# Kernel tuning notes

Measured on AMD Instinct MI355X. Metric: run time of the kernel, lower is better.

The kernel has to match this reference:

```python
import jax, jax.numpy as jnp
import numpy as np

DIM = 128
HEADS = 4
DIM_HEAD = 32
NUM_MEM = 4
H = 256
W = 256
SCALE = DIM_HEAD ** -0.5
NORM_SCALE = DIM ** 0.5


def rms_norm(x, gamma):
    # x: (c, h, w); L2-normalize over channel axis, per spatial location
    x32 = x.astype(jnp.float32)
    n = jnp.linalg.norm(x32, ord=2, axis=0)  # (h, w)
    return (x32 / n * (gamma + 1.0) * NORM_SCALE).astype(x.dtype)


def setup_inputs() -> dict:
    key = jax.random.key(0)
    k0, k1, k2, k3 = jax.random.split(key, 4)
    x = jax.random.normal(k0, (DIM, H, W), dtype=jnp.float32)
    gamma1 = jnp.zeros((DIM, 1, 1), dtype=jnp.float32)
    w_qkv = jax.random.normal(k1, (3 * HEADS * DIM_HEAD, DIM), dtype=jnp.float32) * 0.05
    mem_kv = jax.random.normal(k2, (2, HEADS, DIM_HEAD, NUM_MEM), dtype=jnp.float32)
    w_out = jax.random.normal(k3, (DIM, HEADS * DIM_HEAD), dtype=jnp.float32) * 0.05
    b_out = jnp.zeros((DIM,), dtype=jnp.float32)
    gamma2 = jnp.zeros((DIM, 1, 1), dtype=jnp.float32)
    return {"x": x, "gamma1": gamma1, "w_qkv": w_qkv, "mem_kv": mem_kv,
            "w_out": w_out, "b_out": b_out, "gamma2": gamma2}


def reference(x, gamma1, w_qkv, mem_kv, w_out, b_out, gamma2):
    n = H * W
    xn = rms_norm(x, gamma1)
    # 1x1 conv == channel matmul: (3*hid, c) @ (c, h*w)
    qkv = jnp.einsum('oc,cn->on', w_qkv, xn.reshape(DIM, n))
    q, k, v = jnp.split(qkv, 3, axis=0)
    # (h*d, n) -> (h, d, n)
    q = q.reshape(HEADS, DIM_HEAD, n)
    k = k.reshape(HEADS, DIM_HEAD, n)
    v = v.reshape(HEADS, DIM_HEAD, n)
    mk, mv = mem_kv[0], mem_kv[1]  # (h, d, num_mem)
    k = jnp.concatenate([mk, k], axis=-1)  # (h, d, num_mem + n)
    v = jnp.concatenate([mv, v], axis=-1)
    # softmax over feature dim for q (global max subtract), token dim for k
    q = jax.nn.softmax((q - jnp.max(q)).astype(jnp.float32), axis=-2).astype(q.dtype)
    k = jax.nn.softmax((k - jnp.max(k)).astype(jnp.float32), axis=-1).astype(k.dtype)
    q = q * SCALE
    context = jnp.einsum('hdn,hen->hde', k, v)      # (h, d, d)
    out = jnp.einsum('hde,hdn->hen', context, q)    # (h, d, n)
    out = out.reshape(HEADS * DIM_HEAD, H, W)
    out = jnp.einsum('oc,chw->ohw', w_out, out) + b_out[:, None, None]
    return rms_norm(out, gamma2)
```

## Files before the change

### kernel.cpp

```cpp
#include <hip/hip_runtime.h>
#include <hip/hip_bf16.h>
#include <cstddef>


typedef __attribute__((ext_vector_type(8))) short short8;
typedef __attribute__((ext_vector_type(4))) float f32x4;

static constexpr int   NTOK = 65536;
static constexpr float NORM_SCALE_F = 11.313708498984761f;
static constexpr float SCALE_F      = 0.17677669529663687f;

__device__ __forceinline__ unsigned short f2bf(float f) {
  __hip_bfloat16 h = __float2bfloat16(f);
  return *reinterpret_cast<unsigned short*>(&h);
}
__device__ __forceinline__ short sbf(float f) { return (short)f2bf(f); }

__global__ __launch_bounds__(256) void k0_pack(const float* __restrict__ w_qkv,
                                               const float* __restrict__ gamma1,
                                               unsigned short* __restrict__ Wp) {
  const int id = blockIdx.x * 256 + threadIdx.x;
  const int m = id / 16384, p = id % 16384;
  const int j = p & 7, ln = (p >> 3) & 63, frag = p >> 9;
  const int ks = frag & 3, rt = frag >> 2;
  const int row = rt * 16 + (ln & 15);
  const int c = ks * 32 + (ln >> 4) * 8 + j;
  const float v = w_qkv[(m * 128 + row) * 128 + c] * (gamma1[c] + 1.0f) * NORM_SCALE_F;
  Wp[id] = f2bf(v);
}

__global__ __launch_bounds__(256) void k_norm(const float* __restrict__ x,
                                              unsigned short* __restrict__ xn) {
  const int t = threadIdx.x;
  const int tok = blockIdx.x * 64 + (t >> 2);
  const int cg = (t & 3) * 32;
  float v[32];
  float sq = 0.f;
  #pragma unroll
  for (int j = 0; j < 32; ++j) {
    v[j] = x[(size_t)(cg + j) * NTOK + tok];
    sq += v[j] * v[j];
  }
  sq += __shfl_xor(sq, 1, 64);
  sq += __shfl_xor(sq, 2, 64);
  const float s = rsqrtf(sq);
  #pragma unroll
  for (int g = 0; g < 4; ++g) {
    short8 o;
    #pragma unroll
    for (int j = 0; j < 8; ++j) o[j] = sbf(v[g * 8 + j] * s);
    *reinterpret_cast<short8*>(xn + (size_t)tok * 128 + cg + g * 8) = o;
  }
}

__global__ __launch_bounds__(512) void k1_kv(const unsigned short* __restrict__ xn,
                                             const unsigned short* __restrict__ Wkp,
                                             const unsigned short* __restrict__ Wvp,
                                             float* __restrict__ CpAll) {
  __shared__ float cred[4224];
  const int tid = threadIdx.x, wv = tid >> 6, ln = tid & 63;
  const int g4 = ln >> 4, t16 = ln & 15;
  const int n0 = (blockIdx.x * 8 + wv) * 32;

  for (int i = tid; i < 4224; i += 512) cred[i] = 0.f;
  __syncthreads();

  short8 xf[2][4];
  #pragma unroll
  for (int tg = 0; tg < 2; ++tg)
    #pragma unroll
    for (int ks = 0; ks < 4; ++ks)
      xf[tg][ks] = *reinterpret_cast<const short8*>(
          xn + (size_t)(n0 + tg * 16 + t16) * 128 + ks * 32 + g4 * 8);

  #pragma unroll
  for (int h = 0; h < 4; ++h) {
    f32x4 ka[2][2] = {};
    #pragma unroll
    for (int ks = 0; ks < 4; ++ks) {
      const short8 b0 = *reinterpret_cast<const short8*>(Wkp + (((2 * h + 0) * 4 + ks) * 64 + ln) * 8);
      const short8 b1 = *reinterpret_cast<const short8*>(Wkp + (((2 * h + 1) * 4 + ks) * 64 + ln) * 8);
      #pragma unroll
      for (int tg = 0; tg < 2; ++tg) {
        ka[0][tg] = __builtin_amdgcn_mfma_f32_16x16x32_bf16(xf[tg][ks], b0, ka[0][tg], 0, 0, 0);
        ka[1][tg] = __builtin_amdgcn_mfma_f32_16x16x32_bf16(xf[tg][ks], b1, ka[1][tg], 0, 0, 0);
      }
    }
    short8 keA[2];
    #pragma unroll
    for (int mt = 0; mt < 2; ++mt) {
      float sl = 0.f;
      short8 u;
      #pragma unroll
      for (int tg = 0; tg < 2; ++tg)
        #pragma unroll
        for (int r = 0; r < 4; ++r) {
          const float e = __expf(ka[mt][tg][r]);
          sl += e;
          u[tg * 4 + r] = sbf(e);
        }
      keA[mt] = u;
      sl += __shfl_xor(sl, 16, 64);
      sl += __shfl_xor(sl, 32, 64);
      if (g4 == 0) atomicAdd(&cred[4096 + h * 32 + mt * 16 + t16], sl);
    }
    f32x4 va[2][2] = {};
    #pragma unroll
    for (int ks = 0; ks < 4; ++ks) {
      const short8 b0 = *reinterpret_cast<const short8*>(Wvp + (((2 * h + 0) * 4 + ks) * 64 + ln) * 8);
      const short8 b1 = *reinterpret_cast<const short8*>(Wvp + (((2 * h + 1) * 4 + ks) * 64 + ln) * 8);
      #pragma unroll
      for (int tg = 0; tg < 2; ++tg) {
        va[0][tg] = __builtin_amdgcn_mfma_f32_16x16x32_bf16(xf[tg][ks], b0, va[0][tg], 0, 0, 0);
        va[1][tg] = __builtin_amdgcn_mfma_f32_16x16x32_bf16(xf[tg][ks], b1, va[1][tg], 0, 0, 0);
      }
    }
    short8 vB[2];
    #pragma unroll
    for (int et = 0; et < 2; ++et) {
      short8 u;
      #pragma unroll
      for (int tg = 0; tg < 2; ++tg)
        #pragma unroll
        for (int r = 0; r < 4; ++r)
          u[tg * 4 + r] = sbf(va[et][tg][r]);
      vB[et] = u;
    }
    #pragma unroll
    for (int dt = 0; dt < 2; ++dt)
      #pragma unroll
      for (int et = 0; et < 2; ++et) {
        f32x4 zc = {0.f, 0.f, 0.f, 0.f};
        zc = __builtin_amdgcn_mfma_f32_16x16x32_bf16(keA[dt], vB[et], zc, 0, 0, 0);
        #pragma unroll
        for (int r = 0; r < 4; ++r)
          atomicAdd(&cred[h * 1024 + (dt * 16 + g4 * 4 + r) * 32 + et * 16 + t16], zc[r]);
      }
  }

  __syncthreads();
  for (int i = tid; i < 4224; i += 512)
    CpAll[(size_t)blockIdx.x * 4224 + i] = cred[i];
}

__global__ __launch_bounds__(256) void k3a_reduce(const float* __restrict__ CpAll,
                                                  float* __restrict__ Cpp) {
  __shared__ float red[256];
  const int t = threadIdx.x;
  const int eg = blockIdx.x;
  const int ch = blockIdx.y;
  const int e = eg * 128 + (t & 127);
  const int half = t >> 7;
  float s = 0.f;
  for (int bb = 0; bb < 16; ++bb) {
    const int b = ch * 32 + half * 16 + bb;
    s += CpAll[(size_t)b * 4224 + e];
  }
  red[t] = s;
  __syncthreads();
  if (t < 128) Cpp[ch * 4224 + eg * 128 + t] = red[t] + red[t + 128];
}

__global__ __launch_bounds__(256) void k3b1_ctx(const float* __restrict__ Cpp,
                                                const float* __restrict__ mem_kv,
                                                float* __restrict__ ctx) {
  __shared__ float allv[4224];
  const int t = threadIdx.x;
  for (int e = t; e < 4224; e += 256) {
    float s = 0.f;
    #pragma unroll
    for (int c = 0; c < 8; ++c) s += Cpp[c * 4224 + e];
    allv[e] = s;
  }
  __syncthreads();
  for (int e = t; e < 4224; e += 256) {
    if (e < 4096) {
      const int hh = e >> 10, d = (e >> 5) & 31, ev = e & 31;
      float add = 0.f;
      #pragma unroll
      for (int m = 0; m < 4; ++m)
        add += __expf(mem_kv[(hh * 32 + d) * 4 + m]) * mem_kv[512 + (hh * 32 + ev) * 4 + m];
      allv[e] += add;
    } else {
      const int si = e - 4096;
      const int hh = si >> 5, d = si & 31;
      float add = 0.f;
      #pragma unroll
      for (int m = 0; m < 4; ++m) add += __expf(mem_kv[(hh * 32 + d) * 4 + m]);
      allv[e] += add;
    }
  }
  __syncthreads();
  for (int e = t; e < 4096; e += 256)
    ctx[e] = allv[e] / allv[4096 + (e >> 5)];
}

__global__ __launch_bounds__(256) void k3b2_w2(const float* __restrict__ ctx,
                                               const float* __restrict__ w_out,
                                               unsigned short* __restrict__ W2p) {
  const int base = (blockIdx.x * 256 + threadIdx.x) * 8;
  const int ln = (base >> 3) & 63;
  const int frag = base >> 9;
  const int h = frag & 3, ot = frag >> 2;
  const int o = ot * 16 + (ln & 15);
  float wrow[32];
  #pragma unroll
  for (int e = 0; e < 32; ++e) wrow[e] = w_out[o * 128 + h * 32 + e];
  short8 out8;
  #pragma unroll
  for (int j = 0; j < 8; ++j) {
    const int d = (j >> 2) * 16 + ((ln >> 4) << 2) + (j & 3);
    float s = 0.f;
    #pragma unroll
    for (int e = 0; e < 32; ++e)
      s += wrow[e] * ctx[h * 1024 + d * 32 + e];
    out8[j] = sbf(s * SCALE_F);
  }
  *reinterpret_cast<short8*>(W2p + base) = out8;
}

__global__ __launch_bounds__(256) void k5_out(const unsigned short* __restrict__ xn,
                                              const unsigned short* __restrict__ Wqp,
                                              const unsigned short* __restrict__ W2p,
                                              const float* __restrict__ b_out,
                                              const float* __restrict__ gamma2,
                                              float* __restrict__ y) {
  const int tid = threadIdx.x, wv = tid >> 6, ln = tid & 63;
  const int g4 = ln >> 4, t16 = ln & 15;
  const int n0 = (blockIdx.x * 4 + wv) * 32;

  short8 xf[2][4];
  #pragma unroll
  for (int tg = 0; tg < 2; ++tg)
    #pragma unroll
    for (int ks = 0; ks < 4; ++ks)
      xf[tg][ks] = *reinterpret_cast<const short8*>(
          xn + (size_t)(n0 + tg * 16 + t16) * 128 + ks * 32 + g4 * 8);

  short8 qB[4][2];
  #pragma unroll
  for (int h = 0; h < 4; ++h) {
    f32x4 qa[2][2] = {};
    #pragma unroll
    for (int ks = 0; ks < 4; ++ks) {
      const short8 a0 = *reinterpret_cast<const short8*>(Wqp + (((2 * h + 0) * 4 + ks) * 64 + ln) * 8);
      const short8 a1 = *reinterpret_cast<const short8*>(Wqp + (((2 * h + 1) * 4 + ks) * 64 + ln) * 8);
      #pragma unroll
      for (int tg = 0; tg < 2; ++tg) {
        qa[0][tg] = __builtin_amdgcn_mfma_f32_16x16x32_bf16(a0, xf[tg][ks], qa[0][tg], 0, 0, 0);
        qa[1][tg] = __builtin_amdgcn_mfma_f32_16x16x32_bf16(a1, xf[tg][ks], qa[1][tg], 0, 0, 0);
      }
    }
    #pragma unroll
    for (int tg = 0; tg < 2; ++tg) {
      float ev[2][4];
      float ss = 0.f;
      #pragma unroll
      for (int rtl = 0; rtl < 2; ++rtl)
        #pragma unroll
        for (int r = 0; r < 4; ++r) {
          ev[rtl][r] = __expf(qa[rtl][tg][r]);
          ss += ev[rtl][r];
        }
      ss += __shfl_xor(ss, 16, 64);
      ss += __shfl_xor(ss, 32, 64);
      const float inv = 1.0f / ss;
      short8 u;
      #pragma unroll
      for (int rtl = 0; rtl < 2; ++rtl)
        #pragma unroll
        for (int r = 0; r < 4; ++r)
          u[rtl * 4 + r] = sbf(ev[rtl][r] * inv);
      qB[h][tg] = u;
    }
  }

  f32x4 z[8][2] = {};
  #pragma unroll
  for (int h = 0; h < 4; ++h)
    #pragma unroll
    for (int ot = 0; ot < 8; ++ot) {
      const short8 a = *reinterpret_cast<const short8*>(W2p + ((ot * 4 + h) * 64 + ln) * 8);
      #pragma unroll
      for (int tg = 0; tg < 2; ++tg)
        z[ot][tg] = __builtin_amdgcn_mfma_f32_16x16x32_bf16(a, qB[h][tg], z[ot][tg], 0, 0, 0);
    }

  float ssq[2] = {0.f, 0.f};
  #pragma unroll
  for (int ot = 0; ot < 8; ++ot) {
    const float4 bb = *reinterpret_cast<const float4*>(b_out + ot * 16 + g4 * 4);
    const float barr[4] = {bb.x, bb.y, bb.z, bb.w};
    #pragma unroll
    for (int tg = 0; tg < 2; ++tg)
      #pragma unroll
      for (int r = 0; r < 4; ++r) {
        const float zb = z[ot][tg][r] + barr[r];
        z[ot][tg][r] = zb;
        ssq[tg] += zb * zb;
      }
  }
  float rr[2];
  #pragma unroll
  for (int tg = 0; tg < 2; ++tg) {
    float s = ssq[tg];
    s += __shfl_xor(s, 16, 64);
    s += __shfl_xor(s, 32, 64);
    rr[tg] = rsqrtf(s);
  }
  #pragma unroll
  for (int ot = 0; ot < 8; ++ot) {
    const float4 gg = *reinterpret_cast<const float4*>(gamma2 + ot * 16 + g4 * 4);
    const float garr[4] = {gg.x, gg.y, gg.z, gg.w};
    #pragma unroll
    for (int tg = 0; tg < 2; ++tg)
      #pragma unroll
      for (int r = 0; r < 4; ++r) {
        const int row = ot * 16 + g4 * 4 + r;
        y[(size_t)row * NTOK + n0 + tg * 16 + t16] =
            z[ot][tg][r] * rr[tg] * (garr[r] + 1.0f) * NORM_SCALE_F;
      }
  }
}

extern "C" void kernel_launch(void* const* d_in, const int* in_sizes, int n_in,
                              void* d_out, int out_size, void* d_ws, size_t ws_size,
                              hipStream_t stream) {
  const float* x      = (const float*)d_in[0];
  const float* gamma1 = (const float*)d_in[1];
  const float* w_qkv  = (const float*)d_in[2];
  const float* mem_kv = (const float*)d_in[3];
  const float* w_out  = (const float*)d_in[4];
  const float* b_out  = (const float*)d_in[5];
  const float* gamma2 = (const float*)d_in[6];
  float* out = (float*)d_out;
  float* ws  = (float*)d_ws;

  unsigned short* Wqp = (unsigned short*)ws;
  unsigned short* Wkp = Wqp + 16384;
  unsigned short* Wvp = Wkp + 16384;
  unsigned short* W2p = Wvp + 16384;
  float* CpAll = ws + 32768;
  float* Cpp   = CpAll + 1081344;
  float* ctx   = Cpp + 33792;
  unsigned short* xn = (unsigned short*)(ws + 1152000);

  hipLaunchKernelGGL(k0_pack,    dim3(192),    dim3(256), 0, stream, w_qkv, gamma1, Wqp);
  hipLaunchKernelGGL(k_norm,     dim3(1024),   dim3(256), 0, stream, x, xn);
  hipLaunchKernelGGL(k1_kv,      dim3(256),    dim3(512), 0, stream, xn, Wkp, Wvp, CpAll);
  hipLaunchKernelGGL(k3a_reduce, dim3(33, 8),  dim3(256), 0, stream, CpAll, Cpp);
  hipLaunchKernelGGL(k3b1_ctx,   dim3(1),      dim3(256), 0, stream, Cpp, mem_kv, ctx);
  hipLaunchKernelGGL(k3b2_w2,    dim3(8),      dim3(256), 0, stream, ctx, w_out, W2p);
  hipLaunchKernelGGL(k5_out,     dim3(512),    dim3(256), 0, stream, xn, Wqp, W2p, b_out, gamma2, out);
}
```

Baseline: 182.3 us.

## Fuse all stages into one cooperative persistent kernel with grid syncs

Replaces the seven-kernel pipeline with a single cooperative kernel of 256 blocks that keeps each block's normalized token tile and packed weights in shared memory across phases, using grid.sync between the reduction and context stages. This removes the xn round trip through global memory, the separate weight-pack kernels and several launch gaps. It also accumulates context partials in registers before doing shared atomics once. In exchange, grid-wide barriers serialize the small reduction phases and leave most threads idle during them, and occupancy is limited by the large shared-memory footprint.

```diff
diff --git a/kernel.cpp b/kernel.cpp
--- a/kernel.cpp
+++ b/kernel.cpp
@@ -1,6 +1,9 @@
 #include <hip/hip_runtime.h>
 #include <hip/hip_bf16.h>
+#include <hip/hip_cooperative_groups.h>
 #include <cstddef>
+
+namespace cg = cooperative_groups;
 
 
 typedef __attribute__((ext_vector_type(8))) short short8;
@@ -16,52 +19,65 @@
 }
 __device__ __forceinline__ short sbf(float f) { return (short)f2bf(f); }
 
-__global__ __launch_bounds__(256) void k0_pack(const float* __restrict__ w_qkv,
-                                               const float* __restrict__ gamma1,
-                                               unsigned short* __restrict__ Wp) {
-  const int id = blockIdx.x * 256 + threadIdx.x;
-  const int m = id / 16384, p = id % 16384;
-  const int j = p & 7, ln = (p >> 3) & 63, frag = p >> 9;
-  const int ks = frag & 3, rt = frag >> 2;
-  const int row = rt * 16 + (ln & 15);
-  const int c = ks * 32 + (ln >> 4) * 8 + j;
-  const float v = w_qkv[(m * 128 + row) * 128 + c] * (gamma1[c] + 1.0f) * NORM_SCALE_F;
-  Wp[id] = f2bf(v);
-}
-
-__global__ __launch_bounds__(256) void k_norm(const float* __restrict__ x,
-                                              unsigned short* __restrict__ xn) {
-  const int t = threadIdx.x;
-  const int tok = blockIdx.x * 64 + (t >> 2);
-  const int cg = (t & 3) * 32;
-  float v[32];
-  float sq = 0.f;
-  #pragma unroll
-  for (int j = 0; j < 32; ++j) {
-    v[j] = x[(size_t)(cg + j) * NTOK + tok];
-    sq += v[j] * v[j];
-  }
-  sq += __shfl_xor(sq, 1, 64);
-  sq += __shfl_xor(sq, 2, 64);
-  const float s = rsqrtf(sq);
-  #pragma unroll
-  for (int g = 0; g < 4; ++g) {
+#define MFMA16(A, B, C) __builtin_amdgcn_mfma_f32_16x16x32_bf16((A), (B), (C), 0, 0, 0)
+
+__global__ __launch_bounds__(512, 2) void k_all(
+    const float* __restrict__ x, const float* __restrict__ gamma1,
+    const float* __restrict__ w_qkv, const float* __restrict__ mem_kv,
+    const float* __restrict__ w_out, const float* __restrict__ b_out,
+    const float* __restrict__ gamma2, float* __restrict__ y,
+    float* __restrict__ CpAll, float* __restrict__ Cpp,
+    float* __restrict__ ctxN, unsigned short* __restrict__ W2p) {
+  __shared__ unsigned short xbuf[256 * 136];
+  __shared__ unsigned short wbuf[32768];
+  __shared__ float cred[4224];
+
+  cg::grid_group grid = cg::this_grid();
+
+  const int tid = threadIdx.x, bid = blockIdx.x;
+  const int wv = tid >> 6, ln = tid & 63;
+  const int g4 = ln >> 4, t16 = ln & 15;
+  const int tok0 = bid * 256;
+
+  #pragma unroll
+  for (int g = 0; g < 8; ++g) {
+    const int gi = tid * 8 + g;
+    const int m = 1 + (gi >> 11);
+    const int gg = gi & 2047;
+    const int lnp = gg & 63, frag = gg >> 6;
+    const int ks = frag & 3, rt = frag >> 2;
+    const int row = rt * 16 + (lnp & 15);
+    const int cb = ks * 32 + (lnp >> 4) * 8;
     short8 o;
     #pragma unroll
-    for (int j = 0; j < 8; ++j) o[j] = sbf(v[g * 8 + j] * s);
-    *reinterpret_cast<short8*>(xn + (size_t)tok * 128 + cg + g * 8) = o;
-  }
-}
-
-__global__ __launch_bounds__(512) void k1_kv(const unsigned short* __restrict__ xn,
-                                             const unsigned short* __restrict__ Wkp,
-                                             const unsigned short* __restrict__ Wvp,
-                                             float* __restrict__ CpAll) {
-  __shared__ float cred[4224];
-  const int tid = threadIdx.x, wv = tid >> 6, ln = tid & 63;
-  const int g4 = ln >> 4, t16 = ln & 15;
-  const int n0 = (blockIdx.x * 8 + wv) * 32;
-
+    for (int j = 0; j < 8; ++j)
+      o[j] = sbf(w_qkv[(m * 128 + row) * 128 + cb + j] * (gamma1[cb + j] + 1.0f) * NORM_SCALE_F);
+    *reinterpret_cast<short8*>(&wbuf[gi * 8]) = o;
+  }
+
+  #pragma unroll
+  for (int it = 0; it < 2; ++it) {
+    const int j = it * 512 + tid;
+    const int tl = j >> 2;
+    const int cgs = (j & 3) * 32;
+    float v[32];
+    float sq = 0.f;
+    #pragma unroll
+    for (int jj = 0; jj < 32; ++jj) {
+      v[jj] = x[(size_t)(cgs + jj) * NTOK + tok0 + tl];
+      sq += v[jj] * v[jj];
+    }
+    sq += __shfl_xor(sq, 1, 64);
+    sq += __shfl_xor(sq, 2, 64);
+    const float s = rsqrtf(sq);
+    #pragma unroll
+    for (int g = 0; g < 4; ++g) {
+      short8 o;
+      #pragma unroll
+      for (int jj = 0; jj < 8; ++jj) o[jj] = sbf(v[g * 8 + jj] * s);
+      *reinterpret_cast<short8*>(&xbuf[tl * 136 + cgs + g * 8]) = o;
+    }
+  }
   for (int i = tid; i < 4224; i += 512) cred[i] = 0.f;
   __syncthreads();
 
@@ -71,184 +87,184 @@
     #pragma unroll
     for (int ks = 0; ks < 4; ++ks)
       xf[tg][ks] = *reinterpret_cast<const short8*>(
-          xn + (size_t)(n0 + tg * 16 + t16) * 128 + ks * 32 + g4 * 8);
-
-  #pragma unroll
-  for (int h = 0; h < 4; ++h) {
-    f32x4 ka[2][2] = {};
-    #pragma unroll
-    for (int ks = 0; ks < 4; ++ks) {
-      const short8 b0 = *reinterpret_cast<const short8*>(Wkp + (((2 * h + 0) * 4 + ks) * 64 + ln) * 8);
-      const short8 b1 = *reinterpret_cast<const short8*>(Wkp + (((2 * h + 1) * 4 + ks) * 64 + ln) * 8);
-      #pragma unroll
-      for (int tg = 0; tg < 2; ++tg) {
-        ka[0][tg] = __builtin_amdgcn_mfma_f32_16x16x32_bf16(xf[tg][ks], b0, ka[0][tg], 0, 0, 0);
-        ka[1][tg] = __builtin_amdgcn_mfma_f32_16x16x32_bf16(xf[tg][ks], b1, ka[1][tg], 0, 0, 0);
-      }
-    }
-    short8 keA[2];
-    #pragma unroll
-    for (int mt = 0; mt < 2; ++mt) {
-      float sl = 0.f;
-      short8 u;
-      #pragma unroll
-      for (int tg = 0; tg < 2; ++tg)
-        #pragma unroll
-        for (int r = 0; r < 4; ++r) {
-          const float e = __expf(ka[mt][tg][r]);
-          sl += e;
-          u[tg * 4 + r] = sbf(e);
+          &xbuf[(wv * 32 + tg * 16 + t16) * 136 + ks * 32 + g4 * 8]);
+
+  {
+    f32x4 cacc[4][2][2] = {};
+    float sacc[4][2] = {};
+    #pragma unroll
+    for (int h = 0; h < 4; ++h) {
+      f32x4 ka[2][2] = {};
+      #pragma unroll
+      for (int ks = 0; ks < 4; ++ks) {
+        const short8 b0 = *reinterpret_cast<const short8*>(&wbuf[(((2 * h + 0) * 4 + ks) * 64 + ln) * 8]);
+        const short8 b1 = *reinterpret_cast<const short8*>(&wbuf[(((2 * h + 1) * 4 + ks) * 64 + ln) * 8]);
+        #pragma unroll
+        for (int tg = 0; tg < 2; ++tg) {
+          ka[0][tg] = MFMA16(xf[tg][ks], b0, ka[0][tg]);
+          ka[1][tg] = MFMA16(xf[tg][ks], b1, ka[1][tg]);
         }
-      keA[mt] = u;
-      sl += __shfl_xor(sl, 16, 64);
-      sl += __shfl_xor(sl, 32, 64);
-      if (g4 == 0) atomicAdd(&cred[4096 + h * 32 + mt * 16 + t16], sl);
-    }
-    f32x4 va[2][2] = {};
-    #pragma unroll
-    for (int ks = 0; ks < 4; ++ks) {
-      const short8 b0 = *reinterpret_cast<const short8*>(Wvp + (((2 * h + 0) * 4 + ks) * 64 + ln) * 8);
-      const short8 b1 = *reinterpret_cast<const short8*>(Wvp + (((2 * h + 1) * 4 + ks) * 64 + ln) * 8);
-      #pragma unroll
-      for (int tg = 0; tg < 2; ++tg) {
-        va[0][tg] = __builtin_amdgcn_mfma_f32_16x16x32_bf16(xf[tg][ks], b0, va[0][tg], 0, 0, 0);
-        va[1][tg] = __builtin_amdgcn_mfma_f32_16x16x32_bf16(xf[tg][ks], b1, va[1][tg], 0, 0, 0);
-      }
-    }
-    short8 vB[2];
-    #pragma unroll
-    for (int et = 0; et < 2; ++et) {
-      short8 u;
-      #pragma unroll
-      for (int tg = 0; tg < 2; ++tg)
-        #pragma unroll
-        for (int r = 0; r < 4; ++r)
-          u[tg * 4 + r] = sbf(va[et][tg][r]);
-      vB[et] = u;
-    }
-    #pragma unroll
-    for (int dt = 0; dt < 2; ++dt)
+      }
+      short8 keA[2];
+      #pragma unroll
+      for (int mt = 0; mt < 2; ++mt) {
+        float sl = 0.f;
+        short8 u;
+        #pragma unroll
+        for (int tg = 0; tg < 2; ++tg)
+          #pragma unroll
+          for (int r = 0; r < 4; ++r) {
+            const float e = __expf(ka[mt][tg][r]);
+            sl += e;
+            u[tg * 4 + r] = sbf(e);
+          }
+        keA[mt] = u;
+        sacc[h][mt] += sl;
+      }
+      f32x4 va[2][2] = {};
+      #pragma unroll
+      for (int ks = 0; ks < 4; ++ks) {
+        const short8 b0 = *reinterpret_cast<const short8*>(&wbuf[16384 + (((2 * h + 0) * 4 + ks) * 64 + ln) * 8]);
+        const short8 b1 = *reinterpret_cast<const short8*>(&wbuf[16384 + (((2 * h + 1) * 4 + ks) * 64 + ln) * 8]);
+        #pragma unroll
+        for (int tg = 0; tg < 2; ++tg) {
+          va[0][tg] = MFMA16(xf[tg][ks], b0, va[0][tg]);
+          va[1][tg] = MFMA16(xf[tg][ks], b1, va[1][tg]);
+        }
+      }
+      short8 vB[2];
       #pragma unroll
       for (int et = 0; et < 2; ++et) {
-        f32x4 zc = {0.f, 0.f, 0.f, 0.f};
-        zc = __builtin_amdgcn_mfma_f32_16x16x32_bf16(keA[dt], vB[et], zc, 0, 0, 0);
-        #pragma unroll
-        for (int r = 0; r < 4; ++r)
-          atomicAdd(&cred[h * 1024 + (dt * 16 + g4 * 4 + r) * 32 + et * 16 + t16], zc[r]);
-      }
-  }
-
+        short8 u;
+        #pragma unroll
+        for (int tg = 0; tg < 2; ++tg)
+          #pragma unroll
+          for (int r = 0; r < 4; ++r)
+            u[tg * 4 + r] = sbf(va[et][tg][r]);
+        vB[et] = u;
+      }
+      #pragma unroll
+      for (int dt = 0; dt < 2; ++dt)
+        #pragma unroll
+        for (int et = 0; et < 2; ++et)
+          cacc[h][dt][et] = MFMA16(keA[dt], vB[et], cacc[h][dt][et]);
+    }
+    #pragma unroll
+    for (int h = 0; h < 4; ++h)
+      #pragma unroll
+      for (int dt = 0; dt < 2; ++dt)
+        #pragma unroll
+        for (int et = 0; et < 2; ++et)
+          #pragma unroll
+          for (int r = 0; r < 4; ++r)
+            atomicAdd(&cred[h * 1024 + (dt * 16 + g4 * 4 + r) * 32 + et * 16 + t16],
+                      cacc[h][dt][et][r]);
+    #pragma unroll
+    for (int h = 0; h < 4; ++h)
+      #pragma unroll
+      for (int mt = 0; mt < 2; ++mt) {
+        float sl = sacc[h][mt];
+        sl += __shfl_xor(sl, 16, 64);
+        sl += __shfl_xor(sl, 32, 64);
+        if (g4 == 0) atomicAdd(&cred[4096 + h * 32 + mt * 16 + t16], sl);
+      }
+  }
   __syncthreads();
   for (int i = tid; i < 4224; i += 512)
-    CpAll[(size_t)blockIdx.x * 4224 + i] = cred[i];
-}
-
-__global__ __launch_bounds__(256) void k3a_reduce(const float* __restrict__ CpAll,
-                                                  float* __restrict__ Cpp) {
-  __shared__ float red[256];
-  const int t = threadIdx.x;
-  const int eg = blockIdx.x;
-  const int ch = blockIdx.y;
-  const int e = eg * 128 + (t & 127);
-  const int half = t >> 7;
-  float s = 0.f;
-  for (int bb = 0; bb < 16; ++bb) {
-    const int b = ch * 32 + half * 16 + bb;
-    s += CpAll[(size_t)b * 4224 + e];
-  }
-  red[t] = s;
+    CpAll[(size_t)bid * 4224 + i] = cred[i];
+  __threadfence();
+  grid.sync();
+
+  const int gid = bid * 512 + tid;
+  if (gid < 33792) {
+    const unsigned chunk = (unsigned)gid / 4224u;
+    const unsigned e = (unsigned)gid - chunk * 4224u;
+    float s = 0.f;
+    #pragma unroll 4
+    for (int bb = 0; bb < 32; ++bb)
+      s += CpAll[(size_t)(chunk * 32 + bb) * 4224 + e];
+    Cpp[chunk * 4224 + e] = s;
+  }
+  #pragma unroll
+  for (int g = 0; g < 4; ++g) {
+    const int gi = tid * 4 + g;
+    const int lnp = gi & 63, frag = gi >> 6;
+    const int ks = frag & 3, rt = frag >> 2;
+    const int row = rt * 16 + (lnp & 15);
+    const int cb = ks * 32 + (lnp >> 4) * 8;
+    short8 o;
+    #pragma unroll
+    for (int j = 0; j < 8; ++j)
+      o[j] = sbf(w_qkv[row * 128 + cb + j] * (gamma1[cb + j] + 1.0f) * NORM_SCALE_F);
+    *reinterpret_cast<short8*>(&wbuf[gi * 8]) = o;
+  }
+  __threadfence();
+  grid.sync();
+
+  if (gid < 4224) {
+    float s = 0.f;
+    #pragma unroll
+    for (int c = 0; c < 8; ++c) s += Cpp[c * 4224 + gid];
+    if (gid < 4096) {
+      const int hh = gid >> 10, d = (gid >> 5) & 31, ev = gid & 31;
+      #pragma unroll
+      for (int m = 0; m < 4; ++m)
+        s += __expf(mem_kv[(hh * 32 + d) * 4 + m]) * mem_kv[512 + (hh * 32 + ev) * 4 + m];
+    } else {
+      const int si = gid - 4096;
+      const int hh = si >> 5, d = si & 31;
+      #pragma unroll
+      for (int m = 0; m < 4; ++m) s += __expf(mem_kv[(hh * 32 + d) * 4 + m]);
+    }
+    ctxN[gid] = s;
+  }
+  __threadfence();
+  grid.sync();
+
+  if (gid < 2048) {
+    const int base = gid * 8;
+    const int ln2 = gid & 63, frag = gid >> 6;
+    const int h = frag & 3, ot = frag >> 2;
+    const int o = ot * 16 + (ln2 & 15);
+    float wrow[32];
+    #pragma unroll
+    for (int e = 0; e < 32; ++e) wrow[e] = w_out[o * 128 + h * 32 + e];
+    short8 o8;
+    #pragma unroll
+    for (int j = 0; j < 8; ++j) {
+      const int d = (j >> 2) * 16 + ((ln2 >> 4) << 2) + (j & 3);
+      float s = 0.f;
+      #pragma unroll
+      for (int e = 0; e < 32; ++e)
+        s += wrow[e] * ctxN[h * 1024 + d * 32 + e];
+      o8[j] = sbf(s / ctxN[4096 + h * 32 + d] * SCALE_F);
+    }
+    *reinterpret_cast<short8*>(&W2p[base]) = o8;
+  }
+  __threadfence();
+  grid.sync();
+
+  #pragma unroll
+  for (int g = 0; g < 4; ++g) {
+    const int i8 = (tid * 4 + g) * 8;
+    *reinterpret_cast<short8*>(&wbuf[16384 + i8]) =
+        *reinterpret_cast<const short8*>(&W2p[i8]);
+  }
   __syncthreads();
-  if (t < 128) Cpp[ch * 4224 + eg * 128 + t] = red[t] + red[t + 128];
-}
-
-__global__ __launch_bounds__(256) void k3b1_ctx(const float* __restrict__ Cpp,
-                                                const float* __restrict__ mem_kv,
-                                                float* __restrict__ ctx) {
-  __shared__ float allv[4224];
-  const int t = threadIdx.x;
-  for (int e = t; e < 4224; e += 256) {
-    float s = 0.f;
-    #pragma unroll
-    for (int c = 0; c < 8; ++c) s += Cpp[c * 4224 + e];
-    allv[e] = s;
-  }
-  __syncthreads();
-  for (int e = t; e < 4224; e += 256) {
-    if (e < 4096) {
-      const int hh = e >> 10, d = (e >> 5) & 31, ev = e & 31;
-      float add = 0.f;
-      #pragma unroll
-      for (int m = 0; m < 4; ++m)
-        add += __expf(mem_kv[(hh * 32 + d) * 4 + m]) * mem_kv[512 + (hh * 32 + ev) * 4 + m];
-      allv[e] += add;
-    } else {
-      const int si = e - 4096;
-      const int hh = si >> 5, d = si & 31;
-      float add = 0.f;
-      #pragma unroll
-      for (int m = 0; m < 4; ++m) add += __expf(mem_kv[(hh * 32 + d) * 4 + m]);
-      allv[e] += add;
-    }
-  }
-  __syncthreads();
-  for (int e = t; e < 4096; e += 256)
-    ctx[e] = allv[e] / allv[4096 + (e >> 5)];
-}
-
-__global__ __launch_bounds__(256) void k3b2_w2(const float* __restrict__ ctx,
-                                               const float* __restrict__ w_out,
-                                               unsigned short* __restrict__ W2p) {
-  const int base = (blockIdx.x * 256 + threadIdx.x) * 8;
-  const int ln = (base >> 3) & 63;
-  const int frag = base >> 9;
-  const int h = frag & 3, ot = frag >> 2;
-  const int o = ot * 16 + (ln & 15);
-  float wrow[32];
-  #pragma unroll
-  for (int e = 0; e < 32; ++e) wrow[e] = w_out[o * 128 + h * 32 + e];
-  short8 out8;
-  #pragma unroll
-  for (int j = 0; j < 8; ++j) {
-    const int d = (j >> 2) * 16 + ((ln >> 4) << 2) + (j & 3);
-    float s = 0.f;
-    #pragma unroll
-    for (int e = 0; e < 32; ++e)
-      s += wrow[e] * ctx[h * 1024 + d * 32 + e];
-    out8[j] = sbf(s * SCALE_F);
-  }
-  *reinterpret_cast<short8*>(W2p + base) = out8;
-}
-
-__global__ __launch_bounds__(256) void k5_out(const unsigned short* __restrict__ xn,
-                                              const unsigned short* __restrict__ Wqp,
-                                              const unsigned short* __restrict__ W2p,
-                                              const float* __restrict__ b_out,
-                                              const float* __restrict__ gamma2,
-                                              float* __restrict__ y) {
-  const int tid = threadIdx.x, wv = tid >> 6, ln = tid & 63;
-  const int g4 = ln >> 4, t16 = ln & 15;
-  const int n0 = (blockIdx.x * 4 + wv) * 32;
-
-  short8 xf[2][4];
-  #pragma unroll
-  for (int tg = 0; tg < 2; ++tg)
-    #pragma unroll
-    for (int ks = 0; ks < 4; ++ks)
-      xf[tg][ks] = *reinterpret_cast<const short8*>(
-          xn + (size_t)(n0 + tg * 16 + t16) * 128 + ks * 32 + g4 * 8);
-
+
+  const int n0 = tok0 + wv * 32;
   short8 qB[4][2];
   #pragma unroll
   for (int h = 0; h < 4; ++h) {
     f32x4 qa[2][2] = {};
     #pragma unroll
     for (int ks = 0; ks < 4; ++ks) {
-      const short8 a0 = *reinterpret_cast<const short8*>(Wqp + (((2 * h + 0) * 4 + ks) * 64 + ln) * 8);
-      const short8 a1 = *reinterpret_cast<const short8*>(Wqp + (((2 * h + 1) * 4 + ks) * 64 + ln) * 8);
+      const short8 a0 = *reinterpret_cast<const short8*>(&wbuf[(((2 * h + 0) * 4 + ks) * 64 + ln) * 8]);
+      const short8 a1 = *reinterpret_cast<const short8*>(&wbuf[(((2 * h + 1) * 4 + ks) * 64 + ln) * 8]);
       #pragma unroll
       for (int tg = 0; tg < 2; ++tg) {
-        qa[0][tg] = __builtin_amdgcn_mfma_f32_16x16x32_bf16(a0, xf[tg][ks], qa[0][tg], 0, 0, 0);
-        qa[1][tg] = __builtin_amdgcn_mfma_f32_16x16x32_bf16(a1, xf[tg][ks], qa[1][tg], 0, 0, 0);
+        qa[0][tg] = MFMA16(a0, xf[tg][ks], qa[0][tg]);
+        qa[1][tg] = MFMA16(a1, xf[tg][ks], qa[1][tg]);
       }
     }
     #pragma unroll
@@ -280,10 +296,10 @@
   for (int h = 0; h < 4; ++h)
     #pragma unroll
     for (int ot = 0; ot < 8; ++ot) {
-      const short8 a = *reinterpret_cast<const short8*>(W2p + ((ot * 4 + h) * 64 + ln) * 8);
+      const short8 a = *reinterpret_cast<const short8*>(&wbuf[16384 + ((ot * 4 + h) * 64 + ln) * 8]);
       #pragma unroll
       for (int tg = 0; tg < 2; ++tg)
-        z[ot][tg] = __builtin_amdgcn_mfma_f32_16x16x32_bf16(a, qB[h][tg], z[ot][tg], 0, 0, 0);
+        z[ot][tg] = MFMA16(a, qB[h][tg], z[ot][tg]);
     }
 
   float ssq[2] = {0.f, 0.f};
@@ -336,20 +352,13 @@
   float* out = (float*)d_out;
   float* ws  = (float*)d_ws;
 
-  unsigned short* Wqp = (unsigned short*)ws;
-  unsigned short* Wkp = Wqp + 16384;
-  unsigned short* Wvp = Wkp + 16384;
-  unsigned short* W2p = Wvp + 16384;
-  float* CpAll = ws + 32768;
+  float* CpAll = ws;
   float* Cpp   = CpAll + 1081344;
-  float* ctx   = Cpp + 33792;
-  unsigned short* xn = (unsigned short*)(ws + 1152000);
-
-  hipLaunchKernelGGL(k0_pack,    dim3(192),    dim3(256), 0, stream, w_qkv, gamma1, Wqp);
-  hipLaunchKernelGGL(k_norm,     dim3(1024),   dim3(256), 0, stream, x, xn);
-  hipLaunchKernelGGL(k1_kv,      dim3(256),    dim3(512), 0, stream, xn, Wkp, Wvp, CpAll);
-  hipLaunchKernelGGL(k3a_reduce, dim3(33, 8),  dim3(256), 0, stream, CpAll, Cpp);
-  hipLaunchKernelGGL(k3b1_ctx,   dim3(1),      dim3(256), 0, stream, Cpp, mem_kv, ctx);
-  hipLaunchKernelGGL(k3b2_w2,    dim3(8),      dim3(256), 0, stream, ctx, w_out, W2p);
-  hipLaunchKernelGGL(k5_out,     dim3(512),    dim3(256), 0, stream, xn, Wqp, W2p, b_out, gamma2, out);
+  float* ctxN  = Cpp + 33792;
+  unsigned short* W2p = (unsigned short*)(ctxN + 4224);
+
+  void* args[] = {(void*)&x, (void*)&gamma1, (void*)&w_qkv, (void*)&mem_kv,
+                  (void*)&w_out, (void*)&b_out, (void*)&gamma2, (void*)&out,
+                  (void*)&CpAll, (void*)&Cpp, (void*)&ctxN, (void*)&W2p};
+  hipLaunchCooperativeKernel((const void*)k_all, dim3(256), dim3(512), args, 0, stream);
 }
```

After: 426.9 us. 2.34x slower.

## Fuse weight packing into norm kernel and context into W2 fold, cutting launches

Applied to the files above, without the earlier changes.

Merges the weight-pack kernel into the token-norm kernel as three extra blocks, and merges the single-block context normalization into the W2 folding kernel, where each of the 8 blocks redundantly recomputes the context sums into shared memory. This drops the launch count from seven to five and removes the ctx round-trip through global memory. It also restructures the per-head loops in k1_kv and k5_out with unroll 1, and accumulates the output MFMA inside the head loop so only the current head's q fragments stay live, which lowers register pressure. The cost is some redundant context work per block and less instruction-level parallelism from the non-unrolled head loop.

```diff
diff --git a/kernel.cpp b/kernel.cpp
--- a/kernel.cpp
+++ b/kernel.cpp
@@ -16,40 +16,49 @@
 }
 __device__ __forceinline__ short sbf(float f) { return (short)f2bf(f); }
 
-__global__ __launch_bounds__(256) void k0_pack(const float* __restrict__ w_qkv,
-                                               const float* __restrict__ gamma1,
-                                               unsigned short* __restrict__ Wp) {
-  const int id = blockIdx.x * 256 + threadIdx.x;
-  const int m = id / 16384, p = id % 16384;
-  const int j = p & 7, ln = (p >> 3) & 63, frag = p >> 9;
-  const int ks = frag & 3, rt = frag >> 2;
-  const int row = rt * 16 + (ln & 15);
-  const int c = ks * 32 + (ln >> 4) * 8 + j;
-  const float v = w_qkv[(m * 128 + row) * 128 + c] * (gamma1[c] + 1.0f) * NORM_SCALE_F;
-  Wp[id] = f2bf(v);
-}
-
-__global__ __launch_bounds__(256) void k_norm(const float* __restrict__ x,
-                                              unsigned short* __restrict__ xn) {
-  const int t = threadIdx.x;
-  const int tok = blockIdx.x * 64 + (t >> 2);
-  const int cg = (t & 3) * 32;
-  float v[32];
-  float sq = 0.f;
-  #pragma unroll
-  for (int j = 0; j < 32; ++j) {
-    v[j] = x[(size_t)(cg + j) * NTOK + tok];
-    sq += v[j] * v[j];
-  }
-  sq += __shfl_xor(sq, 1, 64);
-  sq += __shfl_xor(sq, 2, 64);
-  const float s = rsqrtf(sq);
-  #pragma unroll
-  for (int g = 0; g < 4; ++g) {
-    short8 o;
-    #pragma unroll
-    for (int j = 0; j < 8; ++j) o[j] = sbf(v[g * 8 + j] * s);
-    *reinterpret_cast<short8*>(xn + (size_t)tok * 128 + cg + g * 8) = o;
+#define MFMA16(A, B, C) __builtin_amdgcn_mfma_f32_16x16x32_bf16((A), (B), (C), 0, 0, 0)
+
+__global__ __launch_bounds__(256) void k0_norm_pack(const float* __restrict__ x,
+                                                    const float* __restrict__ w_qkv,
+                                                    const float* __restrict__ gamma1,
+                                                    unsigned short* __restrict__ xn,
+                                                    unsigned short* __restrict__ Wall) {
+  const int t = threadIdx.x, bid = blockIdx.x;
+  if (bid < 1024) {
+    const int tok = bid * 64 + (t >> 2);
+    const int cg = (t & 3) * 32;
+    float v[32];
+    float sq = 0.f;
+    #pragma unroll
+    for (int j = 0; j < 32; ++j) {
+      v[j] = x[(size_t)(cg + j) * NTOK + tok];
+      sq += v[j] * v[j];
+    }
+    sq += __shfl_xor(sq, 1, 64);
+    sq += __shfl_xor(sq, 2, 64);
+    const float s = rsqrtf(sq);
+    #pragma unroll
+    for (int g = 0; g < 4; ++g) {
+      short8 o;
+      #pragma unroll
+      for (int j = 0; j < 8; ++j) o[j] = sbf(v[g * 8 + j] * s);
+      *reinterpret_cast<short8*>(xn + (size_t)tok * 128 + cg + g * 8) = o;
+    }
+  } else {
+    const int m = bid - 1024;
+    #pragma unroll
+    for (int g = 0; g < 8; ++g) {
+      const int gi = t * 8 + g;
+      const int lnp = gi & 63, frag = gi >> 6;
+      const int ks = frag & 3, rt = frag >> 2;
+      const int row = rt * 16 + (lnp & 15);
+      const int cb = ks * 32 + (lnp >> 4) * 8;
+      short8 o;
+      #pragma unroll
+      for (int j = 0; j < 8; ++j)
+        o[j] = sbf(w_qkv[(m * 128 + row) * 128 + cb + j] * (gamma1[cb + j] + 1.0f) * NORM_SCALE_F);
+      *reinterpret_cast<short8*>(Wall + m * 16384 + gi * 8) = o;
+    }
   }
 }
 
@@ -73,17 +82,19 @@
       xf[tg][ks] = *reinterpret_cast<const short8*>(
           xn + (size_t)(n0 + tg * 16 + t16) * 128 + ks * 32 + g4 * 8);
 
-  #pragma unroll
+  #pragma unroll 1
   for (int h = 0; h < 4; ++h) {
+    const unsigned short* wk = Wkp + h * 4096;
+    const unsigned short* wvp = Wvp + h * 4096;
     f32x4 ka[2][2] = {};
     #pragma unroll
     for (int ks = 0; ks < 4; ++ks) {
-      const short8 b0 = *reinterpret_cast<const short8*>(Wkp + (((2 * h + 0) * 4 + ks) * 64 + ln) * 8);
-      const short8 b1 = *reinterpret_cast<const short8*>(Wkp + (((2 * h + 1) * 4 + ks) * 64 + ln) * 8);
+      const short8 b0 = *reinterpret_cast<const short8*>(wk + ks * 512 + ln * 8);
+      const short8 b1 = *reinterpret_cast<const short8*>(wk + 2048 + ks * 512 + ln * 8);
       #pragma unroll
       for (int tg = 0; tg < 2; ++tg) {
-        ka[0][tg] = __builtin_amdgcn_mfma_f32_16x16x32_bf16(xf[tg][ks], b0, ka[0][tg], 0, 0, 0);
-        ka[1][tg] = __builtin_amdgcn_mfma_f32_16x16x32_bf16(xf[tg][ks], b1, ka[1][tg], 0, 0, 0);
+        ka[0][tg] = MFMA16(xf[tg][ks], b0, ka[0][tg]);
+        ka[1][tg] = MFMA16(xf[tg][ks], b1, ka[1][tg]);
       }
     }
     short8 keA[2];
@@ -107,12 +118,12 @@
     f32x4 va[2][2] = {};
     #pragma unroll
     for (int ks = 0; ks < 4; ++ks) {
-      const short8 b0 = *reinterpret_cast<const short8*>(Wvp + (((2 * h + 0) * 4 + ks) * 64 + ln) * 8);
-      const short8 b1 = *reinterpret_cast<const short8*>(Wvp + (((2 * h + 1) * 4 + ks) * 64 + ln) * 8);
+      const short8 b0 = *reinterpret_cast<const short8*>(wvp + ks * 512 + ln * 8);
+      const short8 b1 = *reinterpret_cast<const short8*>(wvp + 2048 + ks * 512 + ln * 8);
       #pragma unroll
       for (int tg = 0; tg < 2; ++tg) {
-        va[0][tg] = __builtin_amdgcn_mfma_f32_16x16x32_bf16(xf[tg][ks], b0, va[0][tg], 0, 0, 0);
-        va[1][tg] = __builtin_amdgcn_mfma_f32_16x16x32_bf16(xf[tg][ks], b1, va[1][tg], 0, 0, 0);
+        va[0][tg] = MFMA16(xf[tg][ks], b0, va[0][tg]);
+        va[1][tg] = MFMA16(xf[tg][ks], b1, va[1][tg]);
       }
     }
     short8 vB[2];
@@ -131,7 +142,7 @@
       #pragma unroll
       for (int et = 0; et < 2; ++et) {
         f32x4 zc = {0.f, 0.f, 0.f, 0.f};
-        zc = __builtin_amdgcn_mfma_f32_16x16x32_bf16(keA[dt], vB[et], zc, 0, 0, 0);
+        zc = MFMA16(keA[dt], vB[et], zc);
         #pragma unroll
         for (int r = 0; r < 4; ++r)
           atomicAdd(&cred[h * 1024 + (dt * 16 + g4 * 4 + r) * 32 + et * 16 + t16], zc[r]);
@@ -161,62 +172,49 @@
   if (t < 128) Cpp[ch * 4224 + eg * 128 + t] = red[t] + red[t + 128];
 }
 
-__global__ __launch_bounds__(256) void k3b1_ctx(const float* __restrict__ Cpp,
-                                                const float* __restrict__ mem_kv,
-                                                float* __restrict__ ctx) {
-  __shared__ float allv[4224];
+__global__ __launch_bounds__(256) void k3_ctx_fold(const float* __restrict__ Cpp,
+                                                   const float* __restrict__ mem_kv,
+                                                   const float* __restrict__ w_out,
+                                                   unsigned short* __restrict__ W2p) {
+  __shared__ float ctxs[4224];
   const int t = threadIdx.x;
   for (int e = t; e < 4224; e += 256) {
     float s = 0.f;
     #pragma unroll
     for (int c = 0; c < 8; ++c) s += Cpp[c * 4224 + e];
-    allv[e] = s;
-  }
-  __syncthreads();
-  for (int e = t; e < 4224; e += 256) {
     if (e < 4096) {
       const int hh = e >> 10, d = (e >> 5) & 31, ev = e & 31;
-      float add = 0.f;
       #pragma unroll
       for (int m = 0; m < 4; ++m)
-        add += __expf(mem_kv[(hh * 32 + d) * 4 + m]) * mem_kv[512 + (hh * 32 + ev) * 4 + m];
-      allv[e] += add;
+        s += __expf(mem_kv[(hh * 32 + d) * 4 + m]) * mem_kv[512 + (hh * 32 + ev) * 4 + m];
     } else {
       const int si = e - 4096;
       const int hh = si >> 5, d = si & 31;
-      float add = 0.f;
-      #pragma unroll
-      for (int m = 0; m < 4; ++m) add += __expf(mem_kv[(hh * 32 + d) * 4 + m]);
-      allv[e] += add;
-    }
+      #pragma unroll
+      for (int m = 0; m < 4; ++m) s += __expf(mem_kv[(hh * 32 + d) * 4 + m]);
+    }
+    ctxs[e] = s;
   }
   __syncthreads();
-  for (int e = t; e < 4096; e += 256)
-    ctx[e] = allv[e] / allv[4096 + (e >> 5)];
-}
-
-__global__ __launch_bounds__(256) void k3b2_w2(const float* __restrict__ ctx,
-                                               const float* __restrict__ w_out,
-                                               unsigned short* __restrict__ W2p) {
-  const int base = (blockIdx.x * 256 + threadIdx.x) * 8;
-  const int ln = (base >> 3) & 63;
-  const int frag = base >> 9;
+
+  const int gid = blockIdx.x * 256 + t;
+  const int ln2 = gid & 63, frag = gid >> 6;
   const int h = frag & 3, ot = frag >> 2;
-  const int o = ot * 16 + (ln & 15);
+  const int o = ot * 16 + (ln2 & 15);
   float wrow[32];
   #pragma unroll
   for (int e = 0; e < 32; ++e) wrow[e] = w_out[o * 128 + h * 32 + e];
-  short8 out8;
+  short8 o8;
   #pragma unroll
   for (int j = 0; j < 8; ++j) {
-    const int d = (j >> 2) * 16 + ((ln >> 4) << 2) + (j & 3);
+    const int d = (j >> 2) * 16 + ((ln2 >> 4) << 2) + (j & 3);
     float s = 0.f;
     #pragma unroll
     for (int e = 0; e < 32; ++e)
-      s += wrow[e] * ctx[h * 1024 + d * 32 + e];
-    out8[j] = sbf(s * SCALE_F);
-  }
-  *reinterpret_cast<short8*>(W2p + base) = out8;
+      s += wrow[e] * ctxs[h * 1024 + d * 32 + e];
+    o8[j] = sbf(s / ctxs[4096 + h * 32 + d] * SCALE_F);
+  }
+  *reinterpret_cast<short8*>(W2p + gid * 8) = o8;
 }
 
 __global__ __launch_bounds__(256) void k5_out(const unsigned short* __restrict__ xn,
@@ -237,20 +235,22 @@
       xf[tg][ks] = *reinterpret_cast<const short8*>(
           xn + (size_t)(n0 + tg * 16 + t16) * 128 + ks * 32 + g4 * 8);
 
-  short8 qB[4][2];
-  #pragma unroll
+  f32x4 z[8][2] = {};
+  #pragma unroll 1
   for (int h = 0; h < 4; ++h) {
+    const unsigned short* wq = Wqp + h * 4096;
     f32x4 qa[2][2] = {};
     #pragma unroll
     for (int ks = 0; ks < 4; ++ks) {
-      const short8 a0 = *reinterpret_cast<const short8*>(Wqp + (((2 * h + 0) * 4 + ks) * 64 + ln) * 8);
-      const short8 a1 = *reinterpret_cast<const short8*>(Wqp + (((2 * h + 1) * 4 + ks) * 64 + ln) * 8);
+      const short8 a0 = *reinterpret_cast<const short8*>(wq + ks * 512 + ln * 8);
+      const short8 a1 = *reinterpret_cast<const short8*>(wq + 2048 + ks * 512 + ln * 8);
       #pragma unroll
       for (int tg = 0; tg < 2; ++tg) {
-        qa[0][tg] = __builtin_amdgcn_mfma_f32_16x16x32_bf16(a0, xf[tg][ks], qa[0][tg], 0, 0, 0);
-        qa[1][tg] = __builtin_amdgcn_mfma_f32_16x16x32_bf16(a1, xf[tg][ks], qa[1][tg], 0, 0, 0);
-      }
-    }
+        qa[0][tg] = MFMA16(a0, xf[tg][ks], qa[0][tg]);
+        qa[1][tg] = MFMA16(a1, xf[tg][ks], qa[1][tg]);
+      }
+    }
+    short8 qBl[2];
     #pragma unroll
     for (int tg = 0; tg < 2; ++tg) {
       float ev[2][4];
@@ -271,20 +271,16 @@
         #pragma unroll
         for (int r = 0; r < 4; ++r)
           u[rtl * 4 + r] = sbf(ev[rtl][r] * inv);
-      qB[h][tg] = u;
-    }
-  }
-
-  f32x4 z[8][2] = {};
-  #pragma unroll
-  for (int h = 0; h < 4; ++h)
+      qBl[tg] = u;
+    }
     #pragma unroll
     for (int ot = 0; ot < 8; ++ot) {
       const short8 a = *reinterpret_cast<const short8*>(W2p + ((ot * 4 + h) * 64 + ln) * 8);
       #pragma unroll
       for (int tg = 0; tg < 2; ++tg)
-        z[ot][tg] = __builtin_amdgcn_mfma_f32_16x16x32_bf16(a, qB[h][tg], z[ot][tg], 0, 0, 0);
-    }
+        z[ot][tg] = MFMA16(a, qBl[tg], z[ot][tg]);
+    }
+  }
 
   float ssq[2] = {0.f, 0.f};
   #pragma unroll
@@ -336,20 +332,18 @@
   float* out = (float*)d_out;
   float* ws  = (float*)d_ws;
 
-  unsigned short* Wqp = (unsigned short*)ws;
-  unsigned short* Wkp = Wqp + 16384;
-  unsigned short* Wvp = Wkp + 16384;
-  unsigned short* W2p = Wvp + 16384;
+  unsigned short* Wall = (unsigned short*)ws;
+  unsigned short* Wqp = Wall;
+  unsigned short* Wkp = Wall + 16384;
+  unsigned short* Wvp = Wall + 32768;
+  unsigned short* W2p = (unsigned short*)(ws + 24576);
   float* CpAll = ws + 32768;
   float* Cpp   = CpAll + 1081344;
-  float* ctx   = Cpp + 33792;
-  unsigned short* xn = (unsigned short*)(ws + 1152000);
-
-  hipLaunchKernelGGL(k0_pack,    dim3(192),    dim3(256), 0, stream, w_qkv, gamma1, Wqp);
-  hipLaunchKernelGGL(k_norm,     dim3(1024),   dim3(256), 0, stream, x, xn);
-  hipLaunchKernelGGL(k1_kv,      dim3(256),    dim3(512), 0, stream, xn, Wkp, Wvp, CpAll);
-  hipLaunchKernelGGL(k3a_reduce, dim3(33, 8),  dim3(256), 0, stream, CpAll, Cpp);
-  hipLaunchKernelGGL(k3b1_ctx,   dim3(1),      dim3(256), 0, stream, Cpp, mem_kv, ctx);
-  hipLaunchKernelGGL(k3b2_w2,    dim3(8),      dim3(256), 0, stream, ctx, w_out, W2p);
-  hipLaunchKernelGGL(k5_out,     dim3(512),    dim3(256), 0, stream, xn, Wqp, W2p, b_out, gamma2, out);
-}
+  unsigned short* xn = (unsigned short*)(ws + 1147904);
+
+  hipLaunchKernelGGL(k0_norm_pack, dim3(1027),   dim3(256), 0, stream, x, w_qkv, gamma1, xn, Wall);
+  hipLaunchKernelGGL(k1_kv,        dim3(256),    dim3(512), 0, stream, xn, Wkp, Wvp, CpAll);
+  hipLaunchKernelGGL(k3a_reduce,   dim3(33, 8),  dim3(256), 0, stream, CpAll, Cpp);
+  hipLaunchKernelGGL(k3_ctx_fold,  dim3(8),      dim3(256), 0, stream, Cpp, mem_kv, w_out, W2p);
+  hipLaunchKernelGGL(k5_out,       dim3(512),    dim3(256), 0, stream, xn, Wqp, W2p, b_out, gamma2, out);
+}
```

After: 180.4 us. Within noise of the previous version (-1.0%).
